# Optimization experiments

Hardware: AMD Instinct MI355X
Metric: run time of the kernel (lower is better)

Reference implementation:

```python
import jax, jax.numpy as jnp
import numpy as np

EPS = 1e-6
GROUPS = 32


def setup_inputs() -> dict:
    key = jax.random.key(0)
    ks = jax.random.split(key, 6)
    B, C, T = 4, 256, 4096
    s = 1.0 / np.sqrt(C)
    return {
        "x": jax.random.normal(ks[0], (B, C, T), dtype=jnp.float32),
        "gn_scale": jnp.ones((C,), jnp.float32),
        "gn_bias": jnp.zeros((C,), jnp.float32),
        "wq": jax.random.normal(ks[1], (C, C), jnp.float32) * s,
        "bq": jnp.zeros((C,), jnp.float32),
        "wk": jax.random.normal(ks[2], (C, C), jnp.float32) * s,
        "bk": jnp.zeros((C,), jnp.float32),
        "wv": jax.random.normal(ks[3], (C, C), jnp.float32) * s,
        "bv": jnp.zeros((C,), jnp.float32),
        "wo": jax.random.normal(ks[4], (C, C), jnp.float32) * s,
        "bo": jnp.zeros((C,), jnp.float32),
    }


def _group_norm(x, scale, bias):
    B, C, T = x.shape
    h = x.reshape(B, GROUPS, C // GROUPS, T)
    mean = h.mean(axis=(2, 3), keepdims=True)
    var = ((h - mean) ** 2).mean(axis=(2, 3), keepdims=True)
    h = (h - mean) * jax.lax.rsqrt(var + EPS)
    h = h.reshape(B, C, T)
    return h * scale[None, :, None] + bias[None, :, None]


def _conv1x1(w, b, h):
    # Conv1d kernel_size=1 == per-timestep channel matmul
    return jnp.einsum('oc,bct->bot', w, h) + b[None, :, None]


def reference(x, gn_scale, gn_bias, wq, bq, wk, bk, wv, bv, wo, bo):
    B, C, T = x.shape
    h = _group_norm(x, gn_scale, gn_bias)
    q = _conv1x1(wq, bq, h)  # [B,C,T]
    k = _conv1x1(wk, bk, h)
    v = _conv1x1(wv, bv, h)
    # w_[b,q,k] = sum_c q[b,c,q] k[b,c,k] * C**-0.5, softmax over k
    w = jnp.einsum('bcq,bck->bqk', q, k) * (C ** -0.5)
    w = jax.nn.softmax(w, axis=2)
    # torch code: h_[b, i, c] = sum_j w[b, j, i] * v_perm[b, j, c]
    h = jnp.einsum('bqk,bcq->bck', w, v)  # [B,C,T]
    h = _conv1x1(wo, bo, h)
    return x + h
```

## Files before the change

kernel.cpp:

```cpp
#include <hip/hip_runtime.h>

typedef float f32x4 __attribute__((ext_vector_type(4)));
typedef short s16x8 __attribute__((ext_vector_type(8)));

#define MOFF 12.0f

__device__ __forceinline__ unsigned short f2bf(float f) {
  unsigned int u = __float_as_uint(f);
  u += 0x7fffu + ((u >> 16) & 1u);
  return (unsigned short)(u >> 16);
}

template <typename T>
__device__ __forceinline__ void gload16(const T* g, T* l) {
  __builtin_amdgcn_global_load_lds(
      (const __attribute__((address_space(1))) void*)g,
      (__attribute__((address_space(3))) void*)l, 16, 0, 0);
}

__global__ __launch_bounds__(256) void gn_stats_k(const float* __restrict__ x,
                                                  float* __restrict__ meanv,
                                                  float* __restrict__ rstdv) {
  const int bg = blockIdx.x;
  const float4* base = (const float4*)(x + (size_t)bg * 8 * 4096);
  float s = 0.f, q = 0.f;
  for (int i = threadIdx.x; i < 8192; i += 256) {
    float4 v = base[i];
    s += v.x + v.y + v.z + v.w;
    q += v.x * v.x + v.y * v.y + v.z * v.z + v.w * v.w;
  }
  for (int o = 32; o; o >>= 1) { s += __shfl_down(s, o); q += __shfl_down(q, o); }
  __shared__ float ss[4], sq[4];
  const int wv = threadIdx.x >> 6;
  if ((threadIdx.x & 63) == 0) { ss[wv] = s; sq[wv] = q; }
  __syncthreads();
  if (threadIdx.x == 0) {
    s = ss[0] + ss[1] + ss[2] + ss[3];
    q = sq[0] + sq[1] + sq[2] + sq[3];
    float mu = s * (1.f / 32768.f);
    float var = q * (1.f / 32768.f) - mu * mu;
    meanv[bg] = mu;
    rstdv[bg] = rsqrtf(var + 1e-6f);
  }
}

__global__ __launch_bounds__(256) void gn_apply_t_k(const float* __restrict__ x,
    const float* __restrict__ gamma, const float* __restrict__ beta,
    const float* __restrict__ meanv, const float* __restrict__ rstdv,
    unsigned short* __restrict__ hT) {
  __shared__ unsigned short tile[64][72];
  const int b = blockIdx.z, c0 = blockIdx.y * 64, t0 = blockIdx.x * 64;
  const int tid = threadIdx.x;
  {
    const int tr = tid >> 4, tc = (tid & 15) * 4;
    const float* xb = x + ((size_t)b * 256 + c0) * 4096 + t0;
    for (int p2 = 0; p2 < 4; ++p2) {
      int cl = p2 * 16 + tr;
      int c = c0 + cl;
      int bg = b * 32 + (c >> 3);
      float ga = gamma[c] * rstdv[bg];
      float be = beta[c] - meanv[bg] * ga;
      float4 v = *(const float4*)(xb + (size_t)cl * 4096 + tc);
      tile[cl][tc + 0] = f2bf(v.x * ga + be);
      tile[cl][tc + 1] = f2bf(v.y * ga + be);
      tile[cl][tc + 2] = f2bf(v.z * ga + be);
      tile[cl][tc + 3] = f2bf(v.w * ga + be);
    }
  }
  __syncthreads();
  {
    const int orow = tid >> 3, oc = (tid & 7) * 8;
    unsigned short* hb = hT + ((size_t)b * 4096 + t0) * 256 + c0;
    for (int p2 = 0; p2 < 2; ++p2) {
      int tl = p2 * 32 + orow;
      s16x8 w;
#pragma unroll
      for (int j = 0; j < 8; ++j) w[j] = (short)tile[oc + j][tl];
      *(s16x8*)(hb + (size_t)tl * 256 + oc) = w;
    }
  }
}

enum { EPI_WT = 0, EPI_PB = 1, EPI_FIN = 3 };

template <bool AF32, int EPI>
__global__ __launch_bounds__(256) void gemm64_k(
    const void* __restrict__ Ap, long long sA, int lda,
    const unsigned short* __restrict__ Bp, long long sB, int ldb,
    void* __restrict__ Op, long long sO, int ldo,
    const float* __restrict__ bias,
    const float* __restrict__ xadd, long long sX,
    float scale, int K) {
  __shared__ s16x8 lsA[4][64];
  __shared__ s16x8 lsB[4][64];
  const int tid = threadIdx.x;
  const int m0 = blockIdx.y * 64, n0 = blockIdx.x * 64;
  const int z = blockIdx.z;
  const int lane = tid & 63, wv = tid >> 6;
  const int lrow = lane & 15, lg = lane >> 4;
  const int srow = tid >> 2, scg = tid & 3;
  const int swrow = srow ^ (scg << 1);

  f32x4 acc[4];
#pragma unroll
  for (int i = 0; i < 4; ++i) acc[i] = (f32x4){0.f, 0.f, 0.f, 0.f};

  const unsigned short* Bb = Bp + (size_t)z * sB + (size_t)(n0 + srow) * ldb + scg * 8;

  for (int k0 = 0; k0 < K; k0 += 32) {
    if (AF32) {
      const float* ap = (const float*)Ap + (size_t)z * sA + (size_t)(m0 + srow) * lda + k0 + scg * 8;
      float4 v0 = *(const float4*)ap;
      float4 v1 = *(const float4*)(ap + 4);
      s16x8 w;
      w[0] = (short)f2bf(v0.x); w[1] = (short)f2bf(v0.y);
      w[2] = (short)f2bf(v0.z); w[3] = (short)f2bf(v0.w);
      w[4] = (short)f2bf(v1.x); w[5] = (short)f2bf(v1.y);
      w[6] = (short)f2bf(v1.z); w[7] = (short)f2bf(v1.w);
      lsA[scg][swrow] = w;
    } else {
      const unsigned short* ap = (const unsigned short*)Ap + (size_t)z * sA + (size_t)(m0 + srow) * lda + k0 + scg * 8;
      lsA[scg][swrow] = *(const s16x8*)ap;
    }
    lsB[scg][swrow] = *(const s16x8*)(Bb + k0);
    __syncthreads();
    s16x8 af = lsA[lg][(wv * 16 + lrow) ^ (lg << 1)];
#pragma unroll
    for (int nt = 0; nt < 4; ++nt) {
      s16x8 bf = lsB[lg][(nt * 16 + lrow) ^ (lg << 1)];
      acc[nt] = __builtin_amdgcn_mfma_f32_16x16x32_bf16(af, bf, acc[nt], 0, 0, 0);
    }
    __syncthreads();
  }

  const int mb = m0 + wv * 16 + lg * 4;
  float bv0 = 0.f, bv1 = 0.f, bv2 = 0.f, bv3 = 0.f;
  if (bias) { bv0 = bias[mb]; bv1 = bias[mb + 1]; bv2 = bias[mb + 2]; bv3 = bias[mb + 3]; }
#pragma unroll
  for (int nt = 0; nt < 4; ++nt) {
    const int n = n0 + nt * 16 + lrow;
    if (EPI == EPI_WT) {
      ushort4 pk;
      pk.x = f2bf((acc[nt][0] + bv0) * scale);
      pk.y = f2bf((acc[nt][1] + bv1) * scale);
      pk.z = f2bf((acc[nt][2] + bv2) * scale);
      pk.w = f2bf((acc[nt][3] + bv3) * scale);
      *(ushort4*)((unsigned short*)Op + (size_t)z * sO + (size_t)n * ldo + mb) = pk;
    } else if (EPI == EPI_PB) {
      unsigned short* o = (unsigned short*)Op + (size_t)z * sO;
      o[(size_t)(mb + 0) * ldo + n] = f2bf(acc[nt][0] + bv0);
      o[(size_t)(mb + 1) * ldo + n] = f2bf(acc[nt][1] + bv1);
      o[(size_t)(mb + 2) * ldo + n] = f2bf(acc[nt][2] + bv2);
      o[(size_t)(mb + 3) * ldo + n] = f2bf(acc[nt][3] + bv3);
    } else {
      float* o = (float*)Op + (size_t)z * sO;
      const float* xa = xadd + (size_t)z * sX;
      o[(size_t)(mb + 0) * ldo + n] = acc[nt][0] + bv0 + xa[(size_t)(mb + 0) * ldo + n];
      o[(size_t)(mb + 1) * ldo + n] = acc[nt][1] + bv1 + xa[(size_t)(mb + 1) * ldo + n];
      o[(size_t)(mb + 2) * ldo + n] = acc[nt][2] + bv2 + xa[(size_t)(mb + 2) * ldo + n];
      o[(size_t)(mb + 3) * ldo + n] = acc[nt][3] + bv3 + xa[(size_t)(mb + 3) * ldo + n];
    }
  }
}

__global__ __launch_bounds__(256) void attn_stats3_k(
    const unsigned short* __restrict__ qT,
    const unsigned short* __restrict__ kT,
    float* __restrict__ pl) {
  __shared__ unsigned short kbuf[2][64 * 256];
  const int tid = threadIdx.x;
  const int b = blockIdx.z;
  const int Q0 = blockIdx.x * 256;
  const int kc = blockIdx.y;
  const int lane = tid & 63, wq = tid >> 6;
  const int lrow = lane & 15, lg = lane >> 4;

  const unsigned short* qb = qT + (size_t)b * (4096 * 256);
  const unsigned short* kb = kT + (size_t)b * (4096 * 256);

  s16x8 af[4][8];
#pragma unroll
  for (int mt = 0; mt < 4; ++mt)
#pragma unroll
    for (int ks = 0; ks < 8; ++ks)
      af[mt][ks] = *(const s16x8*)(qb + (size_t)(Q0 + wq * 64 + mt * 16 + lrow) * 256 + ks * 32 + lg * 8);

  float sl[4][4];
#pragma unroll
  for (int mt = 0; mt < 4; ++mt)
#pragma unroll
    for (int j = 0; j < 4; ++j) sl[mt][j] = 0.f;

  int cur = 0;
  {
    const unsigned short* src = kb + (size_t)(kc * 512) * 256;
#pragma unroll
    for (int rep = 0; rep < 8; ++rep) {
      int i = rep * 256 + tid;
      int row = i >> 5, c8 = i & 31;
      gload16(src + (size_t)row * 256 + (c8 ^ (row & 7)) * 8, &kbuf[0][(i - lane) * 8]);
    }
  }
  __syncthreads();

  for (int it = 0; it < 8; ++it) {
    if (it + 1 < 8) {
      const unsigned short* src = kb + (size_t)(kc * 512 + (it + 1) * 64) * 256;
#pragma unroll
      for (int rep = 0; rep < 8; ++rep) {
        int i = rep * 256 + tid;
        int row = i >> 5, c8 = i & 31;
        gload16(src + (size_t)row * 256 + (c8 ^ (row & 7)) * 8, &kbuf[cur ^ 1][(i - lane) * 8]);
      }
    }
#pragma unroll
    for (int nt = 0; nt < 4; ++nt) {
      f32x4 acc[4];
#pragma unroll
      for (int mt = 0; mt < 4; ++mt) acc[mt] = (f32x4){0.f, 0.f, 0.f, 0.f};
#pragma unroll
      for (int ks = 0; ks < 8; ++ks) {
        int row = nt * 16 + lrow;
        int ch = (ks * 4 + lg) ^ (row & 7);
        s16x8 bf = *(const s16x8*)&kbuf[cur][row * 256 + ch * 8];
#pragma unroll
        for (int mt = 0; mt < 4; ++mt)
          acc[mt] = __builtin_amdgcn_mfma_f32_16x16x32_bf16(af[mt][ks], bf, acc[mt], 0, 0, 0);
      }
#pragma unroll
      for (int mt = 0; mt < 4; ++mt)
#pragma unroll
        for (int j = 0; j < 4; ++j) sl[mt][j] += __expf(acc[mt][j] - MOFF);
    }
    __syncthreads();
    cur ^= 1;
  }
#pragma unroll
  for (int mt = 0; mt < 4; ++mt)
#pragma unroll
    for (int j = 0; j < 4; ++j) {
      float v = sl[mt][j];
      v += __shfl_xor(v, 1);
      v += __shfl_xor(v, 2);
      v += __shfl_xor(v, 4);
      v += __shfl_xor(v, 8);
      sl[mt][j] = v;
    }
  if (lrow == 0) {
    float* plb = pl + ((size_t)kc * 4 + b) * 4096;
#pragma unroll
    for (int mt = 0; mt < 4; ++mt)
#pragma unroll
      for (int j = 0; j < 4; ++j)
        plb[Q0 + wq * 64 + mt * 16 + lg * 4 + j] = sl[mt][j];
  }
}

__global__ __launch_bounds__(256) void make_r_k(const float* __restrict__ pl,
                                                float* __restrict__ ra) {
  int i = blockIdx.x * 256 + threadIdx.x;
  int b = i >> 12, q = i & 4095;
  float l = 0.f;
#pragma unroll
  for (int kc = 0; kc < 8; ++kc) l += pl[((size_t)kc * 4 + b) * 4096 + q];
  ra[i] = 1.f / l;
}

__global__ __launch_bounds__(512) void attn_pv7_k(
    const unsigned short* __restrict__ qT,
    const unsigned short* __restrict__ kT,
    const unsigned short* __restrict__ vb,
    const float* __restrict__ ra,
    unsigned short* __restrict__ aT) {
  __shared__ unsigned short qbuf[2][128 * 256];
  __shared__ unsigned short P[64 * 136];
  const int tid = threadIdx.x;
  const int pidx = blockIdx.x;
  const int z = (pidx >> 1) & 3;
  const int kt = ((pidx >> 3) << 1) | (pidx & 1);
  const int K0 = kt * 64;
  const int lane = tid & 63, w = tid >> 6;
  const int lrow = lane & 15, lg = lane >> 4;
  const int khw = w >> 2;
  const int qqw = w & 3;

  const unsigned short* qg = qT + (size_t)z * (4096 * 256);
  const unsigned short* kg = kT + (size_t)z * (4096 * 256);
  const unsigned short* vg = vb + (size_t)z * (4096 * 256);
  const float* rg = ra + (size_t)z * 4096;

  s16x8 kf[2][8];
#pragma unroll
  for (int nt = 0; nt < 2; ++nt)
#pragma unroll
    for (int ks = 0; ks < 8; ++ks)
      kf[nt][ks] = *(const s16x8*)(kg + (size_t)(K0 + khw * 32 + nt * 16 + lrow) * 256 + ks * 32 + lg * 8);

  f32x4 oacc[2][4];
#pragma unroll
  for (int ct = 0; ct < 2; ++ct)
#pragma unroll
    for (int nt = 0; nt < 4; ++nt) oacc[ct][nt] = (f32x4){0.f, 0.f, 0.f, 0.f};

  int cur = 0;
  {
#pragma unroll
    for (int rep = 0; rep < 8; ++rep) {
      int i = rep * 512 + tid;
      int row = i >> 5, c8 = i & 31;
      gload16(qg + (size_t)row * 256 + (c8 ^ (row & 7)) * 8, &qbuf[0][(i - lane) * 8]);
    }
  }
  __syncthreads();

  for (int qi = 0; qi < 32; ++qi) {
    const int q0 = qi * 128;
    s16x8 vf[2][4];
#pragma unroll
    for (int ct = 0; ct < 2; ++ct)
#pragma unroll
      for (int qs = 0; qs < 4; ++qs)
        vf[ct][qs] = *(const s16x8*)(vg + (size_t)(w * 32 + ct * 16 + lrow) * 4096 + q0 + qs * 32 + lg * 8);
    {
      const int qn = ((qi + 1) & 31) * 128;
      const unsigned short* src = qg + (size_t)qn * 256;
#pragma unroll
      for (int rep = 0; rep < 8; ++rep) {
        int i = rep * 512 + tid;
        int row = i >> 5, c8 = i & 31;
        gload16(src + (size_t)row * 256 + (c8 ^ (row & 7)) * 8, &qbuf[cur ^ 1][(i - lane) * 8]);
      }
    }
    f32x4 sacc[2][2];
#pragma unroll
    for (int mt = 0; mt < 2; ++mt)
#pragma unroll
      for (int nt = 0; nt < 2; ++nt) sacc[mt][nt] = (f32x4){0.f, 0.f, 0.f, 0.f};
#pragma unroll
    for (int ks = 0; ks < 8; ++ks) {
      s16x8 qf[2];
#pragma unroll
      for (int mt = 0; mt < 2; ++mt) {
        int row = qqw * 32 + mt * 16 + lrow;
        int ch = (ks * 4 + lg) ^ (row & 7);
        qf[mt] = *(const s16x8*)&qbuf[cur][row * 256 + ch * 8];
      }
#pragma unroll
      for (int mt = 0; mt < 2; ++mt)
#pragma unroll
        for (int nt = 0; nt < 2; ++nt)
          sacc[mt][nt] = __builtin_amdgcn_mfma_f32_16x16x32_bf16(qf[mt], kf[nt][ks], sacc[mt][nt], 0, 0, 0);
    }
#pragma unroll
    for (int mt = 0; mt < 2; ++mt) {
      const int ql = qqw * 32 + mt * 16 + lg * 4;
      const float4 r4 = *(const float4*)(rg + q0 + ql);
#pragma unroll
      for (int nt = 0; nt < 2; ++nt) {
        const int k = khw * 32 + nt * 16 + lrow;
        ushort4 pk;
        pk.x = f2bf(__expf(sacc[mt][nt][0] - MOFF) * r4.x);
        pk.y = f2bf(__expf(sacc[mt][nt][1] - MOFF) * r4.y);
        pk.z = f2bf(__expf(sacc[mt][nt][2] - MOFF) * r4.z);
        pk.w = f2bf(__expf(sacc[mt][nt][3] - MOFF) * r4.w);
        *(ushort4*)&P[k * 136 + ql] = pk;
      }
    }
    asm volatile("s_waitcnt lgkmcnt(0)" ::: "memory");
    __builtin_amdgcn_sched_barrier(0);
    __builtin_amdgcn_s_barrier();
    __builtin_amdgcn_sched_barrier(0);
#pragma unroll
    for (int qs = 0; qs < 4; ++qs) {
      s16x8 pf[4];
#pragma unroll
      for (int nt = 0; nt < 4; ++nt) {
        int k = nt * 16 + lrow;
        pf[nt] = *(const s16x8*)&P[k * 136 + (qs * 4 + lg) * 8];
      }
#pragma unroll
      for (int ct = 0; ct < 2; ++ct)
#pragma unroll
        for (int nt = 0; nt < 4; ++nt)
          oacc[ct][nt] = __builtin_amdgcn_mfma_f32_16x16x32_bf16(vf[ct][qs], pf[nt], oacc[ct][nt], 0, 0, 0);
    }
    asm volatile("s_waitcnt vmcnt(0)" ::: "memory");
    __builtin_amdgcn_sched_barrier(0);
    __builtin_amdgcn_s_barrier();
    __builtin_amdgcn_sched_barrier(0);
    cur ^= 1;
  }
  unsigned short* ab = aT + (size_t)z * (4096 * 256);
#pragma unroll
  for (int ct = 0; ct < 2; ++ct)
#pragma unroll
    for (int nt = 0; nt < 4; ++nt) {
      int k = K0 + nt * 16 + lrow;
      int c = w * 32 + ct * 16 + lg * 4;
      ushort4 pk;
      pk.x = f2bf(oacc[ct][nt][0]);
      pk.y = f2bf(oacc[ct][nt][1]);
      pk.z = f2bf(oacc[ct][nt][2]);
      pk.w = f2bf(oacc[ct][nt][3]);
      *(ushort4*)(ab + (size_t)k * 256 + c) = pk;
    }
}

extern "C" void kernel_launch(void* const* d_in, const int* in_sizes, int n_in,
                              void* d_out, int out_size, void* d_ws, size_t ws_size,
                              hipStream_t stream) {
  const float* x   = (const float*)d_in[0];
  const float* gns = (const float*)d_in[1];
  const float* gnb = (const float*)d_in[2];
  const float* wq  = (const float*)d_in[3];
  const float* bq  = (const float*)d_in[4];
  const float* wk  = (const float*)d_in[5];
  const float* bk  = (const float*)d_in[6];
  const float* wvp = (const float*)d_in[7];
  const float* bv  = (const float*)d_in[8];
  const float* wo  = (const float*)d_in[9];
  const float* bo  = (const float*)d_in[10];
  float* out = (float*)d_out;

  const int B = 4, C = 256, T = 4096;
  const long long TCe = (long long)T * C;

  char* p = (char*)d_ws;
  unsigned short* hT = (unsigned short*)p; p += (size_t)B * TCe * 2;
  unsigned short* qT = (unsigned short*)p; p += (size_t)B * TCe * 2;
  unsigned short* kT = (unsigned short*)p; p += (size_t)B * TCe * 2;
  unsigned short* vb = (unsigned short*)p; p += (size_t)B * TCe * 2;
  unsigned short* aT = (unsigned short*)p; p += (size_t)B * TCe * 2;
  float* gmean = (float*)p; p += 512;
  float* grstd = (float*)p; p += 512;
  float* pl = (float*)p; p += (size_t)8 * B * T * 4;
  float* ra = (float*)p; p += (size_t)B * T * 4;

  gn_stats_k<<<B * 32, 256, 0, stream>>>(x, gmean, grstd);
  gn_apply_t_k<<<dim3(T / 64, C / 64, B), 256, 0, stream>>>(x, gns, gnb, gmean, grstd, hT);

  gemm64_k<true, EPI_WT><<<dim3(T / 64, C / 64, B), 256, 0, stream>>>(
      wq, 0, C, hT, TCe, C, qT, TCe, C, bq, nullptr, 0, 0.0625f, C);
  gemm64_k<true, EPI_WT><<<dim3(T / 64, C / 64, B), 256, 0, stream>>>(
      wk, 0, C, hT, TCe, C, kT, TCe, C, bk, nullptr, 0, 1.0f, C);
  gemm64_k<true, EPI_PB><<<dim3(T / 64, C / 64, B), 256, 0, stream>>>(
      wvp, 0, C, hT, TCe, C, vb, TCe, T, bv, nullptr, 0, 1.0f, C);

  attn_stats3_k<<<dim3(T / 256, 8, B), 256, 0, stream>>>(qT, kT, pl);
  make_r_k<<<B * T / 256, 256, 0, stream>>>(pl, ra);
  attn_pv7_k<<<256, 512, 0, stream>>>(qT, kT, vb, ra, aT);

  gemm64_k<true, EPI_FIN><<<dim3(T / 64, C / 64, B), 256, 0, stream>>>(
      wo, 0, C, aT, TCe, C, out, TCe, T, bo, x, TCe, 1.0f, C);
}
```

Measured before the change: 213.4 us.

## Restructure PV attention kernel to load Q fragments directly into registers

The attention-PV kernel no longer double-buffers Q tiles in LDS through async global-to-LDS loads. Each wave now holds all 64 K rows in registers and loads its own 32 Q rows straight from global memory, processing 256 queries per iteration instead of 128. The P tile is widened and XOR-swizzled to avoid bank conflicts. This frees about 128KB of LDS, which could allow more resident blocks, and halves the barrier count. In exchange it loses the prefetch overlap, puts more pressure on registers, and duplicates K fragment loads across waves.

```diff
diff --git a/kernel.cpp b/kernel.cpp
--- a/kernel.cpp
+++ b/kernel.cpp
@@ -266,14 +266,13 @@
   ra[i] = 1.f / l;
 }
 
-__global__ __launch_bounds__(512) void attn_pv7_k(
+__global__ __launch_bounds__(512) void attn_pv8_k(
     const unsigned short* __restrict__ qT,
     const unsigned short* __restrict__ kT,
     const unsigned short* __restrict__ vb,
     const float* __restrict__ ra,
     unsigned short* __restrict__ aT) {
-  __shared__ unsigned short qbuf[2][128 * 256];
-  __shared__ unsigned short P[64 * 136];
+  __shared__ unsigned short P[64 * 256];
   const int tid = threadIdx.x;
   const int pidx = blockIdx.x;
   const int z = (pidx >> 1) & 3;
@@ -281,20 +280,18 @@
   const int K0 = kt * 64;
   const int lane = tid & 63, w = tid >> 6;
   const int lrow = lane & 15, lg = lane >> 4;
-  const int khw = w >> 2;
-  const int qqw = w & 3;
 
   const unsigned short* qg = qT + (size_t)z * (4096 * 256);
   const unsigned short* kg = kT + (size_t)z * (4096 * 256);
   const unsigned short* vg = vb + (size_t)z * (4096 * 256);
   const float* rg = ra + (size_t)z * 4096;
 
-  s16x8 kf[2][8];
-#pragma unroll
-  for (int nt = 0; nt < 2; ++nt)
-#pragma unroll
-    for (int ks = 0; ks < 8; ++ks)
-      kf[nt][ks] = *(const s16x8*)(kg + (size_t)(K0 + khw * 32 + nt * 16 + lrow) * 256 + ks * 32 + lg * 8);
+  s16x8 kf[4][8];
+#pragma unroll
+  for (int nt = 0; nt < 4; ++nt)
+#pragma unroll
+    for (int ks = 0; ks < 8; ++ks)
+      kf[nt][ks] = *(const s16x8*)(kg + (size_t)(K0 + nt * 16 + lrow) * 256 + ks * 32 + lg * 8);
 
   f32x4 oacc[2][4];
 #pragma unroll
@@ -302,81 +299,76 @@
 #pragma unroll
     for (int nt = 0; nt < 4; ++nt) oacc[ct][nt] = (f32x4){0.f, 0.f, 0.f, 0.f};
 
-  int cur = 0;
-  {
-#pragma unroll
-    for (int rep = 0; rep < 8; ++rep) {
-      int i = rep * 512 + tid;
-      int row = i >> 5, c8 = i & 31;
-      gload16(qg + (size_t)row * 256 + (c8 ^ (row & 7)) * 8, &qbuf[0][(i - lane) * 8]);
-    }
-  }
-  __syncthreads();
-
-  for (int qi = 0; qi < 32; ++qi) {
-    const int q0 = qi * 128;
-    s16x8 vf[2][4];
+  const int qlw = w * 32 + lg * 4;
+  const int sub = qlw & 7;
+
+  for (int qi = 0; qi < 16; ++qi) {
+    const int q0 = qi * 256;
+    float4 r0 = *(const float4*)(rg + q0 + qlw);
+    float4 r1 = *(const float4*)(rg + q0 + qlw + 16);
+    s16x8 qf0[8], qf1[8];
+#pragma unroll
+    for (int ks = 0; ks < 8; ++ks)
+      qf0[ks] = *(const s16x8*)(qg + (size_t)(q0 + w * 32 + lrow) * 256 + ks * 32 + lg * 8);
+#pragma unroll
+    for (int ks = 0; ks < 8; ++ks)
+      qf1[ks] = *(const s16x8*)(qg + (size_t)(q0 + w * 32 + 16 + lrow) * 256 + ks * 32 + lg * 8);
+    f32x4 s0[4];
+#pragma unroll
+    for (int nt = 0; nt < 4; ++nt) s0[nt] = (f32x4){0.f, 0.f, 0.f, 0.f};
+#pragma unroll
+    for (int ks = 0; ks < 8; ++ks)
+#pragma unroll
+      for (int nt = 0; nt < 4; ++nt)
+        s0[nt] = __builtin_amdgcn_mfma_f32_16x16x32_bf16(qf0[ks], kf[nt][ks], s0[nt], 0, 0, 0);
+#pragma unroll
+    for (int nt = 0; nt < 4; ++nt) {
+      const int k = nt * 16 + lrow;
+      const int ch = (qlw >> 3) ^ (k & 7);
+      ushort4 pk;
+      pk.x = f2bf(__expf(s0[nt][0] - MOFF) * r0.x);
+      pk.y = f2bf(__expf(s0[nt][1] - MOFF) * r0.y);
+      pk.z = f2bf(__expf(s0[nt][2] - MOFF) * r0.z);
+      pk.w = f2bf(__expf(s0[nt][3] - MOFF) * r0.w);
+      *(ushort4*)&P[k * 256 + ch * 8 + sub] = pk;
+    }
+    f32x4 s1[4];
+#pragma unroll
+    for (int nt = 0; nt < 4; ++nt) s1[nt] = (f32x4){0.f, 0.f, 0.f, 0.f};
+#pragma unroll
+    for (int ks = 0; ks < 8; ++ks)
+#pragma unroll
+      for (int nt = 0; nt < 4; ++nt)
+        s1[nt] = __builtin_amdgcn_mfma_f32_16x16x32_bf16(qf1[ks], kf[nt][ks], s1[nt], 0, 0, 0);
+#pragma unroll
+    for (int nt = 0; nt < 4; ++nt) {
+      const int k = nt * 16 + lrow;
+      const int ch = ((qlw + 16) >> 3) ^ (k & 7);
+      ushort4 pk;
+      pk.x = f2bf(__expf(s1[nt][0] - MOFF) * r1.x);
+      pk.y = f2bf(__expf(s1[nt][1] - MOFF) * r1.y);
+      pk.z = f2bf(__expf(s1[nt][2] - MOFF) * r1.z);
+      pk.w = f2bf(__expf(s1[nt][3] - MOFF) * r1.w);
+      *(ushort4*)&P[k * 256 + ch * 8 + sub] = pk;
+    }
+    s16x8 vf[2][8];
 #pragma unroll
     for (int ct = 0; ct < 2; ++ct)
 #pragma unroll
-      for (int qs = 0; qs < 4; ++qs)
+      for (int qs = 0; qs < 8; ++qs)
         vf[ct][qs] = *(const s16x8*)(vg + (size_t)(w * 32 + ct * 16 + lrow) * 4096 + q0 + qs * 32 + lg * 8);
-    {
-      const int qn = ((qi + 1) & 31) * 128;
-      const unsigned short* src = qg + (size_t)qn * 256;
-#pragma unroll
-      for (int rep = 0; rep < 8; ++rep) {
-        int i = rep * 512 + tid;
-        int row = i >> 5, c8 = i & 31;
-        gload16(src + (size_t)row * 256 + (c8 ^ (row & 7)) * 8, &qbuf[cur ^ 1][(i - lane) * 8]);
-      }
-    }
-    f32x4 sacc[2][2];
-#pragma unroll
-    for (int mt = 0; mt < 2; ++mt)
-#pragma unroll
-      for (int nt = 0; nt < 2; ++nt) sacc[mt][nt] = (f32x4){0.f, 0.f, 0.f, 0.f};
-#pragma unroll
-    for (int ks = 0; ks < 8; ++ks) {
-      s16x8 qf[2];
-#pragma unroll
-      for (int mt = 0; mt < 2; ++mt) {
-        int row = qqw * 32 + mt * 16 + lrow;
-        int ch = (ks * 4 + lg) ^ (row & 7);
-        qf[mt] = *(const s16x8*)&qbuf[cur][row * 256 + ch * 8];
-      }
-#pragma unroll
-      for (int mt = 0; mt < 2; ++mt)
-#pragma unroll
-        for (int nt = 0; nt < 2; ++nt)
-          sacc[mt][nt] = __builtin_amdgcn_mfma_f32_16x16x32_bf16(qf[mt], kf[nt][ks], sacc[mt][nt], 0, 0, 0);
-    }
-#pragma unroll
-    for (int mt = 0; mt < 2; ++mt) {
-      const int ql = qqw * 32 + mt * 16 + lg * 4;
-      const float4 r4 = *(const float4*)(rg + q0 + ql);
-#pragma unroll
-      for (int nt = 0; nt < 2; ++nt) {
-        const int k = khw * 32 + nt * 16 + lrow;
-        ushort4 pk;
-        pk.x = f2bf(__expf(sacc[mt][nt][0] - MOFF) * r4.x);
-        pk.y = f2bf(__expf(sacc[mt][nt][1] - MOFF) * r4.y);
-        pk.z = f2bf(__expf(sacc[mt][nt][2] - MOFF) * r4.z);
-        pk.w = f2bf(__expf(sacc[mt][nt][3] - MOFF) * r4.w);
-        *(ushort4*)&P[k * 136 + ql] = pk;
-      }
-    }
     asm volatile("s_waitcnt lgkmcnt(0)" ::: "memory");
     __builtin_amdgcn_sched_barrier(0);
     __builtin_amdgcn_s_barrier();
     __builtin_amdgcn_sched_barrier(0);
 #pragma unroll
-    for (int qs = 0; qs < 4; ++qs) {
+    for (int qs = 0; qs < 8; ++qs) {
       s16x8 pf[4];
 #pragma unroll
       for (int nt = 0; nt < 4; ++nt) {
-        int k = nt * 16 + lrow;
-        pf[nt] = *(const s16x8*)&P[k * 136 + (qs * 4 + lg) * 8];
+        const int k = nt * 16 + lrow;
+        const int ch = (qs * 4 + lg) ^ (k & 7);
+        pf[nt] = *(const s16x8*)&P[k * 256 + ch * 8];
       }
 #pragma unroll
       for (int ct = 0; ct < 2; ++ct)
@@ -384,11 +376,9 @@
         for (int nt = 0; nt < 4; ++nt)
           oacc[ct][nt] = __builtin_amdgcn_mfma_f32_16x16x32_bf16(vf[ct][qs], pf[nt], oacc[ct][nt], 0, 0, 0);
     }
-    asm volatile("s_waitcnt vmcnt(0)" ::: "memory");
     __builtin_amdgcn_sched_barrier(0);
     __builtin_amdgcn_s_barrier();
     __builtin_amdgcn_sched_barrier(0);
-    cur ^= 1;
   }
   unsigned short* ab = aT + (size_t)z * (4096 * 256);
 #pragma unroll
@@ -448,7 +438,7 @@
 
   attn_stats3_k<<<dim3(T / 256, 8, B), 256, 0, stream>>>(qT, kT, pl);
   make_r_k<<<B * T / 256, 256, 0, stream>>>(pl, ra);
-  attn_pv7_k<<<256, 512, 0, stream>>>(qT, kT, vb, ra, aT);
+  attn_pv8_k<<<256, 512, 0, stream>>>(qT, kT, vb, ra, aT);
 
   gemm64_k<true, EPI_FIN><<<dim3(T / 64, C / 64, B), 256, 0, stream>>>(
       wo, 0, C, aT, TCe, C, out, TCe, T, bo, x, TCe, 1.0f, C);
```

New measurement: 247.6 us. +16.0%, slower.

## Retile attention PV kernel to 32-key tiles with 256-thread blocks at two per CU

Applied to the files above, without the earlier changes.

The attention PV kernel is rebuilt around 32-key tiles, 64-query chunks and 4 waves per block, launched as 512 blocks of 256 threads with two blocks per CU. The S matmul is transposed so each wave owns 16 queries and all 32 keys, and P gets an XOR-swizzled layout in place of padding to avoid LDS bank conflicts. Shared memory per block drops, so occupancy can rise and the grid fills more CUs. In exchange the Q stream is re-read by twice as many blocks and each block does twice as many loop iterations with more barriers.

```diff
diff --git a/kernel.cpp b/kernel.cpp
--- a/kernel.cpp
+++ b/kernel.cpp
@@ -266,23 +266,22 @@
   ra[i] = 1.f / l;
 }
 
-__global__ __launch_bounds__(512) void attn_pv7_k(
+__global__ __launch_bounds__(256, 2) void attn_pv11_k(
     const unsigned short* __restrict__ qT,
     const unsigned short* __restrict__ kT,
     const unsigned short* __restrict__ vb,
     const float* __restrict__ ra,
     unsigned short* __restrict__ aT) {
-  __shared__ unsigned short qbuf[2][128 * 256];
-  __shared__ unsigned short P[64 * 136];
+  __shared__ unsigned short qbuf[2][64 * 256];
+  __shared__ unsigned short P[32 * 64];
   const int tid = threadIdx.x;
   const int pidx = blockIdx.x;
   const int z = (pidx >> 1) & 3;
   const int kt = ((pidx >> 3) << 1) | (pidx & 1);
-  const int K0 = kt * 64;
+  const int K0 = kt * 32;
   const int lane = tid & 63, w = tid >> 6;
   const int lrow = lane & 15, lg = lane >> 4;
-  const int khw = w >> 2;
-  const int qqw = w & 3;
+  const int l7 = lrow & 7;
 
   const unsigned short* qg = qT + (size_t)z * (4096 * 256);
   const unsigned short* kg = kT + (size_t)z * (4096 * 256);
@@ -294,94 +293,82 @@
   for (int nt = 0; nt < 2; ++nt)
 #pragma unroll
     for (int ks = 0; ks < 8; ++ks)
-      kf[nt][ks] = *(const s16x8*)(kg + (size_t)(K0 + khw * 32 + nt * 16 + lrow) * 256 + ks * 32 + lg * 8);
-
-  f32x4 oacc[2][4];
-#pragma unroll
-  for (int ct = 0; ct < 2; ++ct)
-#pragma unroll
-    for (int nt = 0; nt < 4; ++nt) oacc[ct][nt] = (f32x4){0.f, 0.f, 0.f, 0.f};
+      kf[nt][ks] = *(const s16x8*)(kg + (size_t)(K0 + nt * 16 + lrow) * 256 + ks * 32 + lg * 8);
+
+  f32x4 oacc[4][2];
+#pragma unroll
+  for (int ct = 0; ct < 4; ++ct)
+#pragma unroll
+    for (int nt = 0; nt < 2; ++nt) oacc[ct][nt] = (f32x4){0.f, 0.f, 0.f, 0.f};
 
   int cur = 0;
   {
 #pragma unroll
     for (int rep = 0; rep < 8; ++rep) {
-      int i = rep * 512 + tid;
+      int i = rep * 256 + tid;
       int row = i >> 5, c8 = i & 31;
       gload16(qg + (size_t)row * 256 + (c8 ^ (row & 7)) * 8, &qbuf[0][(i - lane) * 8]);
     }
   }
   __syncthreads();
 
-  for (int qi = 0; qi < 32; ++qi) {
-    const int q0 = qi * 128;
-    s16x8 vf[2][4];
-#pragma unroll
-    for (int ct = 0; ct < 2; ++ct)
-#pragma unroll
-      for (int qs = 0; qs < 4; ++qs)
-        vf[ct][qs] = *(const s16x8*)(vg + (size_t)(w * 32 + ct * 16 + lrow) * 4096 + q0 + qs * 32 + lg * 8);
+  for (int qi = 0; qi < 64; ++qi) {
+    const int q0 = qi * 64;
+    s16x8 vf[4][2];
+#pragma unroll
+    for (int ct = 0; ct < 4; ++ct)
+#pragma unroll
+      for (int qs = 0; qs < 2; ++qs)
+        vf[ct][qs] = *(const s16x8*)(vg + (size_t)(w * 64 + ct * 16 + lrow) * 4096 + q0 + qs * 32 + lg * 8);
+    const float rv = rg[q0 + w * 16 + lrow];
     {
-      const int qn = ((qi + 1) & 31) * 128;
+      const int qn = ((qi + 1) & 63) * 64;
       const unsigned short* src = qg + (size_t)qn * 256;
 #pragma unroll
       for (int rep = 0; rep < 8; ++rep) {
-        int i = rep * 512 + tid;
+        int i = rep * 256 + tid;
         int row = i >> 5, c8 = i & 31;
         gload16(src + (size_t)row * 256 + (c8 ^ (row & 7)) * 8, &qbuf[cur ^ 1][(i - lane) * 8]);
       }
     }
-    f32x4 sacc[2][2];
-#pragma unroll
-    for (int mt = 0; mt < 2; ++mt)
-#pragma unroll
-      for (int nt = 0; nt < 2; ++nt) sacc[mt][nt] = (f32x4){0.f, 0.f, 0.f, 0.f};
+    f32x4 sacc[2];
+    sacc[0] = (f32x4){0.f, 0.f, 0.f, 0.f};
+    sacc[1] = (f32x4){0.f, 0.f, 0.f, 0.f};
 #pragma unroll
     for (int ks = 0; ks < 8; ++ks) {
-      s16x8 qf[2];
-#pragma unroll
-      for (int mt = 0; mt < 2; ++mt) {
-        int row = qqw * 32 + mt * 16 + lrow;
-        int ch = (ks * 4 + lg) ^ (row & 7);
-        qf[mt] = *(const s16x8*)&qbuf[cur][row * 256 + ch * 8];
-      }
-#pragma unroll
-      for (int mt = 0; mt < 2; ++mt)
-#pragma unroll
-        for (int nt = 0; nt < 2; ++nt)
-          sacc[mt][nt] = __builtin_amdgcn_mfma_f32_16x16x32_bf16(qf[mt], kf[nt][ks], sacc[mt][nt], 0, 0, 0);
-    }
-#pragma unroll
-    for (int mt = 0; mt < 2; ++mt) {
-      const int ql = qqw * 32 + mt * 16 + lg * 4;
-      const float4 r4 = *(const float4*)(rg + q0 + ql);
-#pragma unroll
-      for (int nt = 0; nt < 2; ++nt) {
-        const int k = khw * 32 + nt * 16 + lrow;
-        ushort4 pk;
-        pk.x = f2bf(__expf(sacc[mt][nt][0] - MOFF) * r4.x);
-        pk.y = f2bf(__expf(sacc[mt][nt][1] - MOFF) * r4.y);
-        pk.z = f2bf(__expf(sacc[mt][nt][2] - MOFF) * r4.z);
-        pk.w = f2bf(__expf(sacc[mt][nt][3] - MOFF) * r4.w);
-        *(ushort4*)&P[k * 136 + ql] = pk;
-      }
+      const int ch = (ks * 4 + lg) ^ l7;
+      s16x8 qf = *(const s16x8*)&qbuf[cur][(w * 16 + lrow) * 256 + ch * 8];
+      sacc[0] = __builtin_amdgcn_mfma_f32_16x16x32_bf16(kf[0][ks], qf, sacc[0], 0, 0, 0);
+      sacc[1] = __builtin_amdgcn_mfma_f32_16x16x32_bf16(kf[1][ks], qf, sacc[1], 0, 0, 0);
+    }
+    {
+      const int q = w * 16 + lrow;
+      const int qc = (q >> 3);
+      const int qs7 = q & 7;
+#pragma unroll
+      for (int nt = 0; nt < 2; ++nt)
+#pragma unroll
+        for (int j = 0; j < 4; ++j) {
+          const int k = nt * 16 + lg * 4 + j;
+          P[k * 64 + ((qc ^ (k & 7)) << 3) + qs7] = f2bf(__expf(sacc[nt][j] - MOFF) * rv);
+        }
     }
     asm volatile("s_waitcnt lgkmcnt(0)" ::: "memory");
     __builtin_amdgcn_sched_barrier(0);
     __builtin_amdgcn_s_barrier();
     __builtin_amdgcn_sched_barrier(0);
 #pragma unroll
-    for (int qs = 0; qs < 4; ++qs) {
-      s16x8 pf[4];
-#pragma unroll
-      for (int nt = 0; nt < 4; ++nt) {
-        int k = nt * 16 + lrow;
-        pf[nt] = *(const s16x8*)&P[k * 136 + (qs * 4 + lg) * 8];
+    for (int qs = 0; qs < 2; ++qs) {
+      s16x8 pf[2];
+#pragma unroll
+      for (int nt = 0; nt < 2; ++nt) {
+        const int k = nt * 16 + lrow;
+        pf[nt] = *(const s16x8*)&P[k * 64 + (((qs * 4 + lg) ^ (k & 7)) << 3)];
       }
 #pragma unroll
-      for (int ct = 0; ct < 2; ++ct)
-#pragma unroll
-        for (int nt = 0; nt < 4; ++nt)
+      for (int ct = 0; ct < 4; ++ct)
+#pragma unroll
+        for (int nt = 0; nt < 2; ++nt)
           oacc[ct][nt] = __builtin_amdgcn_mfma_f32_16x16x32_bf16(vf[ct][qs], pf[nt], oacc[ct][nt], 0, 0, 0);
     }
     asm volatile("s_waitcnt vmcnt(0)" ::: "memory");
@@ -392,11 +379,11 @@
   }
   unsigned short* ab = aT + (size_t)z * (4096 * 256);
 #pragma unroll
-  for (int ct = 0; ct < 2; ++ct)
-#pragma unroll
-    for (int nt = 0; nt < 4; ++nt) {
+  for (int ct = 0; ct < 4; ++ct)
+#pragma unroll
+    for (int nt = 0; nt < 2; ++nt) {
       int k = K0 + nt * 16 + lrow;
-      int c = w * 32 + ct * 16 + lg * 4;
+      int c = w * 64 + ct * 16 + lg * 4;
       ushort4 pk;
       pk.x = f2bf(oacc[ct][nt][0]);
       pk.y = f2bf(oacc[ct][nt][1]);
@@ -448,7 +435,7 @@
 
   attn_stats3_k<<<dim3(T / 256, 8, B), 256, 0, stream>>>(qT, kT, pl);
   make_r_k<<<B * T / 256, 256, 0, stream>>>(pl, ra);
-  attn_pv7_k<<<256, 512, 0, stream>>>(qT, kT, vb, ra, aT);
+  attn_pv11_k<<<512, 256, 0, stream>>>(qT, kT, vb, ra, aT);
 
   gemm64_k<true, EPI_FIN><<<dim3(T / 64, C / 64, B), 256, 0, stream>>>(
       wo, 0, C, aT, TCe, C, out, TCe, T, bo, x, TCe, 1.0f, C);
```

Measured after the change: 257.4 us. +20.6%, slower.
